# Performance work log

Hardware: AMD Instinct MI355X
Metric: run time of the kernel (lower is better)

Reference implementation:

```python
import jax, jax.numpy as jnp
import numpy as np

D = 2            # stalk dimension d
FD = 3           # final_d = d + 1 (add_lp=True, add_hp=False)
HID = 32         # hidden_channels
N_NODES = 50000
E0 = 200000      # undirected edges; directed edge list has 2*E0 entries (second half reversed)
IN_CH = 128
OUT_CH = 32
N_LAYERS = 2
PSIZE = D * (D + 1) // 2  # cayley param size per edge


def _spectral_normalize(W, iters=20):
    # torch spectral_norm: power iteration with detached u, v; sigma = u^T W v
    u = jnp.full((W.shape[0],), 1.0 / np.sqrt(W.shape[0]), W.dtype)
    def body(_, u):
        v = W.T @ u
        v = v / (jnp.linalg.norm(v) + 1e-12)
        u2 = W @ v
        return u2 / (jnp.linalg.norm(u2) + 1e-12)
    u = jax.lax.fori_loop(0, iters, body, u)
    u = jax.lax.stop_gradient(u)
    v = jax.lax.stop_gradient(W.T @ u)
    v = v / (jnp.linalg.norm(v) + 1e-12)
    return W / (u @ W @ v)


def _cayley(p):
    # p: [E, PSIZE] lower-tri params -> skew A -> orthogonal Q = (I - A)^{-1}(I + A)
    E = p.shape[0]
    r, c = jnp.tril_indices(D)
    M = jnp.zeros((E, D, D), p.dtype).at[:, r, c].set(p)
    A = M - jnp.swapaxes(M, 1, 2)
    I = jnp.eye(D, dtype=p.dtype)
    return jnp.linalg.solve(I[None] - A, I[None] + A)


def setup_inputs() -> dict:
    key = jax.random.key(0)
    ks = jax.random.split(key, 8)
    src = jax.random.randint(ks[0], (E0,), 0, N_NODES)
    dst = jax.random.randint(ks[1], (E0,), 0, N_NODES)
    # symmetric directed edge list; edge j and edge j+E0 are reverses of each other
    edge_index = jnp.concatenate([jnp.stack([src, dst]), jnp.stack([dst, src])], axis=1)
    x = jax.random.normal(ks[2], (N_NODES, IN_CH), jnp.float32)
    s = 0.02
    W1 = jax.random.normal(ks[3], (FD * HID, IN_CH), jnp.float32) * s
    b1 = jnp.zeros((FD * HID,), jnp.float32)
    W2 = jax.random.normal(ks[4], (OUT_CH, FD * HID), jnp.float32) * s
    b2 = jnp.zeros((OUT_CH,), jnp.float32)
    W_left = jnp.tile(jnp.eye(FD, dtype=jnp.float32)[None], (N_LAYERS, 1, 1))  # init eye per torch
    W_right = jax.random.normal(ks[5], (N_LAYERS, HID, HID), jnp.float32) / np.sqrt(HID)
    eps = jnp.zeros((N_LAYERS, FD, 1), jnp.float32)
    W_sheaf = jax.random.normal(ks[6], (N_LAYERS, PSIZE, 2 * FD * HID), jnp.float32) * s
    W_wt = jax.random.normal(ks[7], (N_LAYERS, 1, 2 * FD * HID), jnp.float32) * s
    return {"x": x, "edge_index": edge_index, "W1": W1, "b1": b1, "W2": W2, "b2": b2,
            "W_left": W_left, "W_right": W_right, "eps": eps, "W_sheaf": W_sheaf, "W_wt": W_wt}


def reference(x, edge_index, W1, b1, W2, b2, W_left, W_right, eps, W_sheaf, W_wt):
    N = x.shape[0]
    row, col = edge_index[0], edge_index[1]
    e0 = row.shape[0] // 2
    rev = jnp.concatenate([jnp.arange(e0) + e0, jnp.arange(e0)])  # reverse-edge index
    # lin1 + ELU (dropouts = 0 in eval)
    h = jax.nn.elu(x @ W1.T + b1)                 # [N, FD*HID]
    xc = h.reshape(N * FD, HID)                   # [N*FD, HID]
    x0 = xc
    for layer in range(N_LAYERS):
        # --- sheaf learner + edge weight learner (gather endpoint features) ---
        xn = xc.reshape(N, FD * HID)
        cat = jnp.concatenate([xn[row], xn[col]], axis=-1)   # [2*E0, 2*FD*HID]
        p = jnp.tanh(cat @ W_sheaf[layer].T)                 # sheaf map params [2*E0, PSIZE]
        wdir = jax.nn.sigmoid(cat @ W_wt[layer].T)[:, 0]
        w = wdir * wdir[rev]                                 # symmetric edge weight
        # --- normalized connection (bundle) Laplacian ---
        Q = _cayley(p)                                       # per-edge orthogonal maps
        T = jnp.einsum('eij,eik->ejk', Q, Q[rev])            # transport F_u^T F_v
        w2 = w * w
        deg = jax.ops.segment_sum(w2, row, num_segments=N)
        dinv = jnp.where(deg > 0, jax.lax.rsqrt(jnp.maximum(deg, 1e-30)), 0.0)
        cnorm = w2 * dinv[row] * dinv[col]                   # [2*E0]
        # --- left / right weights (spectral-normalized) ---
        Wl = _spectral_normalize(W_left[layer])
        Wr = _spectral_normalize(W_right[layer])
        y = xc.reshape(N, FD, HID)
        y = jnp.einsum('ef,nfh->neh', Wl, y)                 # mix stalk dims
        y = jnp.einsum('neh,ch->nec', y, Wr)                 # mix channels
        # --- apply block-sparse Laplacian: Lx[u] = x[u] - sum_e c_e B_e x[v] ---
        yv = y[col]                                          # gather  [2*E0, FD, HID]
        tv = jnp.concatenate([jnp.einsum('eij,ejh->eih', T, yv[:, :D]), yv[:, D:]], axis=1)
        agg = jax.ops.segment_sum(cnorm[:, None, None] * tv, row, num_segments=N)
        diag = jnp.where(deg > 0, 1.0, 0.0)[:, None, None]
        z = jax.nn.elu((diag * y - agg).reshape(N * FD, HID))
        # --- epsilon-gated residual ---
        coeff = jnp.tile(1.0 + jnp.tanh(eps[layer]), (N, 1))  # [N*FD, 1]
        x0 = coeff * x0 - z
        xc = x0
    return xc.reshape(N, FD * HID) @ W2.T + b2
```

## Files before the change

### kernel.cpp

```cpp
#include <hip/hip_runtime.h>
#include <hip/hip_bf16.h>

#define NN   50000
#define E0   200000
#define E2   400000

typedef __attribute__((ext_vector_type(8))) short short8;
typedef __attribute__((ext_vector_type(4))) float f32x4;

__device__ __forceinline__ float eluf(float x) { return x > 0.0f ? x : expm1f(x); }
__device__ __forceinline__ float sigmoidf(float x) { return 1.0f / (1.0f + expf(-x)); }
__device__ __forceinline__ unsigned rne_bf16(float x) {
    unsigned u = __float_as_uint(x);
    return (u + 0x7fffu + ((u >> 16) & 1u)) >> 16;
}

__global__ __launch_bounds__(256) void k_splitw(const float* __restrict__ W, int n,
                                                unsigned short* __restrict__ hi,
                                                unsigned short* __restrict__ lo) {
    int i = blockIdx.x * 256 + threadIdx.x;
    if (i >= n) return;
    float x = W[i];
    unsigned h = rne_bf16(x);
    hi[i] = (unsigned short)h;
    lo[i] = (unsigned short)rne_bf16(x - __uint_as_float(h << 16));
}

template<int K, int N, bool ELU>
__global__ __launch_bounds__(256) void k_gemm_mfma(const float* __restrict__ X,
                                                   const unsigned short* __restrict__ Whi,
                                                   const unsigned short* __restrict__ Wlo,
                                                   const float* __restrict__ bias,
                                                   float* __restrict__ out) {
    constexpr int KP = K + 8;
    constexpr int NT = N / 16;
    constexpr int KS = K / 32;
    __shared__ __align__(16) unsigned short whi[N * KP];
    __shared__ __align__(16) unsigned short wlo[N * KP];
    int tid = threadIdx.x;
    for (int i = tid; i < N * K / 2; i += 256) {
        unsigned vh = ((const unsigned*)Whi)[i];
        unsigned vl = ((const unsigned*)Wlo)[i];
        int e = i * 2, r = e / K, c = e % K;
        *(unsigned*)&whi[r * KP + c] = vh;
        *(unsigned*)&wlo[r * KP + c] = vl;
    }
    __syncthreads();
    int wave = tid >> 6, lane = tid & 63;
    int quad = lane >> 4, r16 = lane & 15;
    long m = (long)blockIdx.x * 64 + wave * 16 + r16;
    long mc = m < NN ? m : (NN - 1);
    const float* xrow = X + mc * K + quad * 8;
    f32x4 acc[NT];
#pragma unroll
    for (int t = 0; t < NT; ++t) acc[t] = (f32x4){0.f, 0.f, 0.f, 0.f};
#pragma unroll
    for (int ks = 0; ks < KS; ++ks) {
        const float4* xp = (const float4*)(xrow + ks * 32);
        float4 p0 = xp[0], p1 = xp[1];
        float xv[8] = {p0.x, p0.y, p0.z, p0.w, p1.x, p1.y, p1.z, p1.w};
        short8 a_hi, a_lo;
#pragma unroll
        for (int j = 0; j < 8; ++j) {
            unsigned h = rne_bf16(xv[j]);
            a_hi[j] = (short)h;
            a_lo[j] = (short)rne_bf16(xv[j] - __uint_as_float(h << 16));
        }
#pragma unroll
        for (int t = 0; t < NT; ++t) {
            int ro = (t * 16 + r16) * KP + ks * 32 + quad * 8;
            short8 bh = *(const short8*)&whi[ro];
            short8 bl = *(const short8*)&wlo[ro];
            acc[t] = __builtin_amdgcn_mfma_f32_16x16x32_bf16(a_hi, bh, acc[t], 0, 0, 0);
            acc[t] = __builtin_amdgcn_mfma_f32_16x16x32_bf16(a_lo, bh, acc[t], 0, 0, 0);
            acc[t] = __builtin_amdgcn_mfma_f32_16x16x32_bf16(a_hi, bl, acc[t], 0, 0, 0);
        }
    }
    long mbase = (long)blockIdx.x * 64 + wave * 16 + quad * 4;
#pragma unroll
    for (int t = 0; t < NT; ++t) {
        float b = bias[t * 16 + r16];
#pragma unroll
        for (int rr = 0; rr < 4; ++rr) {
            long mm = mbase + rr;
            if (mm < NN) {
                float v = acc[t][rr] + b;
                if (ELU) v = eluf(v);
                out[mm * N + t * 16 + r16] = v;
            }
        }
    }
}

__global__ __launch_bounds__(64) void k_spectral(const float* __restrict__ Wl_in,
                                                 const float* __restrict__ Wr_in,
                                                 float* __restrict__ Wl_out,
                                                 float* __restrict__ Wr_out) {
    int l = blockIdx.x, t = threadIdx.x;
    __shared__ float W[32 * 33];
    __shared__ float us[32], vs[32], tmp[32];
    __shared__ float scal;
    for (int i = t; i < 1024; i += 64) W[(i >> 5) * 33 + (i & 31)] = Wr_in[l * 1024 + i];
    if (t < 32) us[t] = 0.17677669529663688f;
    __syncthreads();
    for (int it = 0; it < 20; ++it) {
        if (t < 32) { float a = 0; for (int r = 0; r < 32; ++r) a = fmaf(W[r * 33 + t], us[r], a); tmp[t] = a; }
        __syncthreads();
        if (t == 0) { float s = 0; for (int c = 0; c < 32; ++c) s += tmp[c] * tmp[c]; scal = 1.0f / (sqrtf(s) + 1e-12f); }
        __syncthreads();
        if (t < 32) vs[t] = tmp[t] * scal;
        __syncthreads();
        if (t < 32) { float a = 0; for (int c = 0; c < 32; ++c) a = fmaf(W[t * 33 + c], vs[c], a); tmp[t] = a; }
        __syncthreads();
        if (t == 0) { float s = 0; for (int r = 0; r < 32; ++r) s += tmp[r] * tmp[r]; scal = 1.0f / (sqrtf(s) + 1e-12f); }
        __syncthreads();
        if (t < 32) us[t] = tmp[t] * scal;
        __syncthreads();
    }
    if (t < 32) { float a = 0; for (int r = 0; r < 32; ++r) a = fmaf(W[r * 33 + t], us[r], a); tmp[t] = a; }
    __syncthreads();
    if (t == 0) {
        float s = 0; for (int c = 0; c < 32; ++c) s += tmp[c] * tmp[c];
        scal = (sqrtf(s) + 1e-12f) / s;
    }
    __syncthreads();
    for (int i = t; i < 1024; i += 64) Wr_out[l * 1024 + i] = W[(i >> 5) * 33 + (i & 31)] * scal;

    if (t == 0) {
        float M[9];
        for (int i = 0; i < 9; ++i) M[i] = Wl_in[l * 9 + i];
        float u[3] = {0.5773502691896258f, 0.5773502691896258f, 0.5773502691896258f};
        float v[3], u2[3];
        for (int it = 0; it < 20; ++it) {
            float s = 0;
            for (int c = 0; c < 3; ++c) { v[c] = M[c] * u[0] + M[3 + c] * u[1] + M[6 + c] * u[2]; s += v[c] * v[c]; }
            float inv = 1.0f / (sqrtf(s) + 1e-12f);
            for (int c = 0; c < 3; ++c) v[c] *= inv;
            s = 0;
            for (int r = 0; r < 3; ++r) { u2[r] = M[r * 3] * v[0] + M[r * 3 + 1] * v[1] + M[r * 3 + 2] * v[2]; s += u2[r] * u2[r]; }
            inv = 1.0f / (sqrtf(s) + 1e-12f);
            for (int r = 0; r < 3; ++r) u[r] = u2[r] * inv;
        }
        float s = 0;
        for (int c = 0; c < 3; ++c) { v[c] = M[c] * u[0] + M[3 + c] * u[1] + M[6 + c] * u[2]; s += v[c] * v[c]; }
        float inv = (sqrtf(s) + 1e-12f) / s;
        for (int i = 0; i < 9; ++i) Wl_out[l * 9 + i] = M[i] * inv;
    }
}

__global__ __launch_bounds__(256) void k_hist(const int* __restrict__ row, int* __restrict__ cnt) {
    int e = blockIdx.x * 256 + threadIdx.x;
    if (e < E2) atomicAdd(&cnt[row[e]], 1);
}
__global__ __launch_bounds__(256) void k_scan1(const int* __restrict__ cnt, int* __restrict__ start,
                                               int* __restrict__ bsum) {
    __shared__ int s[256];
    int b = blockIdx.x, t = threadIdx.x;
    int i = b * 256 + t;
    int v = (i < NN) ? cnt[i] : 0;
    s[t] = v;
    __syncthreads();
    for (int off = 1; off < 256; off <<= 1) {
        int add = (t >= off) ? s[t - off] : 0;
        __syncthreads();
        s[t] += add;
        __syncthreads();
    }
    if (i < NN) start[i] = s[t] - v;
    if (t == 255) bsum[b] = s[t];
}
__global__ __launch_bounds__(256) void k_scan2(const int* __restrict__ bsum, int* __restrict__ bofs,
                                               int nb) {
    __shared__ int s[256];
    int t = threadIdx.x;
    int v = (t < nb) ? bsum[t] : 0;
    s[t] = v;
    __syncthreads();
    for (int off = 1; off < 256; off <<= 1) {
        int add = (t >= off) ? s[t - off] : 0;
        __syncthreads();
        s[t] += add;
        __syncthreads();
    }
    if (t < nb) bofs[t] = s[t] - v;
}
__global__ __launch_bounds__(256) void k_scan3(int* __restrict__ start, const int* __restrict__ bofs) {
    int i = blockIdx.x * 256 + threadIdx.x;
    if (i < NN) start[i] += bofs[i >> 8];
}
__global__ __launch_bounds__(256) void k_fill(const int* __restrict__ row, const int* __restrict__ start,
                                              int* __restrict__ fill, int* __restrict__ eslot) {
    int e = blockIdx.x * 256 + threadIdx.x;
    if (e >= E2) return;
    int u = row[e];
    eslot[e] = start[u] + atomicAdd(&fill[u], 1);
}

__global__ __launch_bounds__(256) void k_y8(const float* __restrict__ xc,
                                            const float* __restrict__ Wl,
                                            const float* __restrict__ Wr,
                                            const float* __restrict__ Wsh,
                                            const float* __restrict__ Wwt,
                                            int layer,
                                            unsigned* __restrict__ yp01,
                                            unsigned short* __restrict__ yp2,
                                            float* __restrict__ aR, float* __restrict__ aC,
                                            float* __restrict__ wR, float* __restrict__ wC,
                                            float* __restrict__ deg) {
    __shared__ float wrs[32 * 33];
    __shared__ float wls[9];
    __shared__ float xcs[8][96];
    __shared__ float ws1[192], wt[192];
    int tid = threadIdx.x;
    int n0 = blockIdx.x * 8;
    if (tid < 8) { int nz = n0 + tid; if (nz < NN) deg[nz] = 0.0f; }
    for (int i = tid; i < 1024; i += 256) wrs[(i >> 5) * 33 + (i & 31)] = Wr[i];
    if (tid < 9) wls[tid] = Wl[tid];
    if (tid < 192) {
        ws1[tid] = Wsh[(layer * 3 + 1) * 192 + tid];
        wt[tid]  = Wwt[layer * 192 + tid];
    }
    for (int i = tid; i < 768; i += 256) {
        int n = n0 + i / 96;
        xcs[i / 96][i % 96] = (n < NN) ? xc[n * 96 + i % 96] : 0.0f;
    }
    __syncthreads();
    int node = tid >> 5, c = tid & 31;
    int n = n0 + node;
    float a1 = 0, a2 = 0, a3 = 0, a4 = 0;
#pragma unroll
    for (int j = 0; j < 3; ++j) {
        int k = j * 32 + c;
        float xv = xcs[node][k];
        a1 = fmaf(xv, ws1[k], a1);
        a2 = fmaf(xv, ws1[96 + k], a2);
        a3 = fmaf(xv, wt[k], a3);
        a4 = fmaf(xv, wt[96 + k], a4);
    }
#pragma unroll
    for (int off = 16; off; off >>= 1) {
        a1 += __shfl_xor(a1, off);
        a2 += __shfl_xor(a2, off);
        a3 += __shfl_xor(a3, off);
        a4 += __shfl_xor(a4, off);
    }
    if (c == 0 && n < NN) { aR[n] = a1; aC[n] = a2; wR[n] = a3; wC[n] = a4; }
    if (n < NN) {
        float t0 = 0, t1 = 0, t2 = 0;
        const float* wr = &wrs[c * 33];
        const float* xr = xcs[node];
#pragma unroll
        for (int h = 0; h < 32; ++h) {
            float w = wr[h];
            t0 = fmaf(xr[h], w, t0);
            t1 = fmaf(xr[32 + h], w, t1);
            t2 = fmaf(xr[64 + h], w, t2);
        }
        float o0 = wls[0] * t0 + wls[1] * t1 + wls[2] * t2;
        float o1 = wls[3] * t0 + wls[4] * t1 + wls[5] * t2;
        float o2 = wls[6] * t0 + wls[7] * t1 + wls[8] * t2;
        yp01[n * 32 + c] = rne_bf16(o0) | (rne_bf16(o1) << 16);
        yp2[n * 32 + c]  = (unsigned short)rne_bf16(o2);
    }
}

__global__ __launch_bounds__(256) void k_edge_coef(const int* __restrict__ row, const int* __restrict__ col,
                                                   const int* __restrict__ eslot,
                                                   const float* __restrict__ aR, const float* __restrict__ aC,
                                                   const float* __restrict__ wR, const float* __restrict__ wC,
                                                   float4* __restrict__ meta, float* __restrict__ deg) {
    int e = blockIdx.x * 256 + threadIdx.x;
    if (e >= E0) return;
    int u = row[e], v = col[e];
    float a_e = tanhf(aR[u] + aC[v]);
    float a_r = tanhf(aR[v] + aC[u]);
    float wd_e = sigmoidf(wR[u] + wC[v]);
    float wd_r = sigmoidf(wR[v] + wC[u]);
    float w = wd_e * wd_r;
    float w2 = w * w;
    float ie = 1.0f / (1.0f + a_e * a_e), ir = 1.0f / (1.0f + a_r * a_r);
    float ce = (1.0f - a_e * a_e) * ie, se = 2.0f * a_e * ie;
    float cr = (1.0f - a_r * a_r) * ir, sr = 2.0f * a_r * ir;
    float C = ce * cr + se * sr;
    float S = ce * sr - se * cr;
    meta[eslot[e]]      = make_float4(C,  S, w2, __int_as_float(v));
    meta[eslot[e + E0]] = make_float4(C, -S, w2, __int_as_float(u));
    atomicAdd(&deg[u], w2);
    atomicAdd(&deg[v], w2);
}

__global__ __launch_bounds__(256) void k_dinv(const float* __restrict__ deg, float* __restrict__ dinv) {
    int n = blockIdx.x * 256 + threadIdx.x;
    if (n >= NN) return;
    float d = deg[n];
    dinv[n] = d > 0.0f ? rsqrtf(fmaxf(d, 1e-30f)) : 0.0f;
}

__global__ __launch_bounds__(256) void k_gather_update(const int* __restrict__ start, const int* __restrict__ cnt,
                                                       const float4* __restrict__ meta,
                                                       const float* __restrict__ dinv,
                                                       const unsigned* __restrict__ yp01,
                                                       const unsigned short* __restrict__ yp2,
                                                       const float* __restrict__ eps,
                                                       int layer, float* __restrict__ xc) {
    int tid = threadIdx.x;
    int node = tid >> 5, c = tid & 31;
    int n = blockIdx.x * 8 + node;
    if (n >= NN) return;
    int s0 = start[n], ec = cnt[n];
    float du = dinv[n];
    float acc0 = 0, acc1 = 0, acc2 = 0;
    for (int bs = 0; bs < ec; bs += 32) {
        int nb = min(32, ec - bs);
        float CC = 0, SS = 0, cnl = 0;
        int vj = 0;
        if (c < nb) {
            float4 mt = meta[s0 + bs + c];
            vj = __float_as_int(mt.w);
            cnl = mt.z * du * dinv[vj];
            CC = cnl * mt.x;
            SS = cnl * mt.y;
        }
        for (int j = 0; j < nb; ++j) {
            float Cj = __shfl(CC, j, 32);
            float Sj = __shfl(SS, j, 32);
            float cj = __shfl(cnl, j, 32);
            int v = __shfl(vj, j, 32);
            unsigned u01 = yp01[v * 32 + c];
            unsigned u2v = (unsigned)yp2[v * 32 + c];
            float y0 = __uint_as_float(u01 << 16);
            float y1 = __uint_as_float(u01 & 0xffff0000u);
            float y2 = __uint_as_float(u2v << 16);
            acc0 = fmaf(Cj, y0, acc0);
            acc0 = fmaf(-Sj, y1, acc0);
            acc1 = fmaf(Sj, y0, acc1);
            acc1 = fmaf(Cj, y1, acc1);
            acc2 = fmaf(cj, y2, acc2);
        }
    }
    float diag = du > 0.0f ? 1.0f : 0.0f;
    unsigned u01 = yp01[n * 32 + c];
    unsigned u2v = (unsigned)yp2[n * 32 + c];
    float oy0 = __uint_as_float(u01 << 16);
    float oy1 = __uint_as_float(u01 & 0xffff0000u);
    float oy2 = __uint_as_float(u2v << 16);
    float c0 = 1.0f + tanhf(eps[layer * 3 + 0]);
    float c1 = 1.0f + tanhf(eps[layer * 3 + 1]);
    float c2 = 1.0f + tanhf(eps[layer * 3 + 2]);
    int base = n * 96 + c;
    float z0 = eluf(diag * oy0 - acc0);
    float z1 = eluf(diag * oy1 - acc1);
    float z2 = eluf(diag * oy2 - acc2);
    xc[base]      = c0 * xc[base]      - z0;
    xc[base + 32] = c1 * xc[base + 32] - z1;
    xc[base + 64] = c2 * xc[base + 64] - z2;
}

extern "C" void kernel_launch(void* const* d_in, const int* in_sizes, int n_in,
                              void* d_out, int out_size, void* d_ws, size_t ws_size,
                              hipStream_t stream) {
    const float* x     = (const float*)d_in[0];
    const int*   ei    = (const int*)d_in[1];
    const float* W1    = (const float*)d_in[2];
    const float* b1    = (const float*)d_in[3];
    const float* W2    = (const float*)d_in[4];
    const float* bias2 = (const float*)d_in[5];
    const float* Wl_in = (const float*)d_in[6];
    const float* Wr_in = (const float*)d_in[7];
    const float* eps   = (const float*)d_in[8];
    const float* Wsh   = (const float*)d_in[9];
    const float* Wwt   = (const float*)d_in[10];
    float* out = (float*)d_out;
    const int* row = ei;
    const int* col = ei + E2;

    char* pc = (char*)d_ws;
    float* xc    = (float*)pc;          pc += (size_t)NN * 96 * 4;
    float4* meta = (float4*)pc;         pc += (size_t)E2 * 16;
    unsigned* yp01 = (unsigned*)pc;     pc += (size_t)NN * 32 * 4;
    unsigned short* yp2 = (unsigned short*)pc; pc += (size_t)NN * 32 * 2;
    float* aR    = (float*)pc;          pc += (size_t)NN * 4;
    float* aC    = (float*)pc;          pc += (size_t)NN * 4;
    float* wRp   = (float*)pc;          pc += (size_t)NN * 4;
    float* wCp   = (float*)pc;          pc += (size_t)NN * 4;
    float* deg   = (float*)pc;          pc += (size_t)NN * 4;
    float* dinv  = (float*)pc;          pc += (size_t)NN * 4;
    float* Wl_n  = (float*)pc;          pc += 32 * 4;
    float* Wr_n  = (float*)pc;          pc += 2048 * 4;
    int* cnt     = (int*)pc;            pc += (size_t)NN * 4;
    int* start   = (int*)pc;            pc += (size_t)NN * 4;
    int* fill    = (int*)pc;            pc += (size_t)NN * 4;
    int* eslot   = (int*)pc;            pc += (size_t)E2 * 4;
    int* bsum    = (int*)pc;            pc += 256 * 4;
    int* bofs    = (int*)pc;            pc += 256 * 4;
    unsigned short* w1hi = (unsigned short*)pc; pc += 96 * 128 * 2;
    unsigned short* w1lo = (unsigned short*)pc; pc += 96 * 128 * 2;
    unsigned short* w2hi = (unsigned short*)pc; pc += 32 * 96 * 2;
    unsigned short* w2lo = (unsigned short*)pc; pc += 32 * 96 * 2;

    const int NB  = (NN + 255) / 256;
    const int EB  = (E2 + 255) / 256;
    const int EB0 = (E0 + 255) / 256;
    const int MB  = (NN + 63) / 64;

    k_splitw<<<(96 * 128 + 255) / 256, 256, 0, stream>>>(W1, 96 * 128, w1hi, w1lo);
    k_splitw<<<(32 * 96 + 255) / 256, 256, 0, stream>>>(W2, 32 * 96, w2hi, w2lo);
    k_gemm_mfma<128, 96, true><<<MB, 256, 0, stream>>>(x, w1hi, w1lo, b1, xc);
    k_spectral<<<2, 64, 0, stream>>>(Wl_in, Wr_in, Wl_n, Wr_n);

    hipMemsetAsync(cnt, 0, NN * sizeof(int), stream);
    hipMemsetAsync(fill, 0, NN * sizeof(int), stream);
    k_hist<<<EB, 256, 0, stream>>>(row, cnt);
    k_scan1<<<NB, 256, 0, stream>>>(cnt, start, bsum);
    k_scan2<<<1, 256, 0, stream>>>(bsum, bofs, NB);
    k_scan3<<<NB, 256, 0, stream>>>(start, bofs);
    k_fill<<<EB, 256, 0, stream>>>(row, start, fill, eslot);

    for (int l = 0; l < 2; ++l) {
        k_y8<<<(NN + 7) / 8, 256, 0, stream>>>(xc, Wl_n + l * 9, Wr_n + l * 1024, Wsh, Wwt, l,
                                               yp01, yp2, aR, aC, wRp, wCp, deg);
        k_edge_coef<<<EB0, 256, 0, stream>>>(row, col, eslot, aR, aC, wRp, wCp, meta, deg);
        k_dinv<<<NB, 256, 0, stream>>>(deg, dinv);
        k_gather_update<<<(NN + 7) / 8, 256, 0, stream>>>(start, cnt, meta, dinv,
                                                          yp01, yp2, eps, l, xc);
    }
    k_gemm_mfma<96, 32, false><<<MB, 256, 0, stream>>>(xc, w2hi, w2lo, bias2, out);
}
```

Baseline: 377.6 us.

## Fuse all stages into one persistent cooperative kernel with grid syncs

Replaces the sequence of about 20 kernel launches (weight split, GEMMs, spectral norm, CSR build, per-layer edge/gather passes) with a single cooperative persistent kernel that separates the phases with grid.sync, and keeps the old multi-kernel path as a fallback. The aim is to remove launch overhead and inter-kernel gaps. The GEMM is restructured to stage 16-row weight slices in a shared-memory union, which adds block barriers and repeated weight loads per tile. Spectral normalisation is overlapped with the first GEMM on two dedicated blocks. Occupancy is capped by launch_bounds(256,4), and many grid-wide syncs plus reduced parallelism in some phases may offset the savings.

```diff
diff --git a/kernel.cpp b/kernel.cpp
--- a/kernel.cpp
+++ b/kernel.cpp
@@ -1,12 +1,17 @@
 #include <hip/hip_runtime.h>
-#include <hip/hip_bf16.h>
-
-#define NN   50000
-#define E0   200000
-#define E2   400000
+#include <hip/hip_cooperative_groups.h>
+
+#define NN 50000
+#define E0 200000
+#define E2 400000
+#define NGROUPS ((NN + 7) / 8)
+#define NCHUNK  ((NN + 255) / 256)
+#define NTILES  ((NN + 63) / 64)
 
 typedef __attribute__((ext_vector_type(8))) short short8;
 typedef __attribute__((ext_vector_type(4))) float f32x4;
+
+namespace cg = cooperative_groups;
 
 __device__ __forceinline__ float eluf(float x) { return x > 0.0f ? x : expm1f(x); }
 __device__ __forceinline__ float sigmoidf(float x) { return 1.0f / (1.0f + expf(-x)); }
@@ -15,117 +20,122 @@
     return (u + 0x7fffu + ((u >> 16) & 1u)) >> 16;
 }
 
-__global__ __launch_bounds__(256) void k_splitw(const float* __restrict__ W, int n,
-                                                unsigned short* __restrict__ hi,
-                                                unsigned short* __restrict__ lo) {
-    int i = blockIdx.x * 256 + threadIdx.x;
-    if (i >= n) return;
-    float x = W[i];
-    unsigned h = rne_bf16(x);
-    hi[i] = (unsigned short)h;
-    lo[i] = (unsigned short)rne_bf16(x - __uint_as_float(h << 16));
-}
+struct SMemGemm { unsigned short whi[16 * 136]; unsigned short wlo[16 * 136]; };
+struct SMemY8   { float wrs[32 * 33]; float wls[9]; float xcs[8][96]; float ws1[192]; float wt[192]; };
+struct SMemSpec { float W[32 * 33]; float us[32]; float vs[32]; float tmp[32]; float scal; };
+struct SMemScan { int s[256]; };
+union SMem { SMemGemm g; SMemY8 y; SMemSpec sp; SMemScan sc; };
+
+struct Params {
+    const float* x; const int* ei;
+    const float *W1, *b1, *W2, *b2, *Wl, *Wr, *eps, *Wsh, *Wwt;
+    float* out;
+    float* xc; float4* meta; unsigned* yp01; unsigned short* yp2;
+    float *aR, *aC, *wR, *wC, *deg, *dinv, *Wl_n, *Wr_n;
+    int *cnt, *start, *fill, *eslot, *bsum, *bofs;
+    unsigned short *w1hi, *w1lo, *w2hi, *w2lo;
+};
 
 template<int K, int N, bool ELU>
-__global__ __launch_bounds__(256) void k_gemm_mfma(const float* __restrict__ X,
-                                                   const unsigned short* __restrict__ Whi,
-                                                   const unsigned short* __restrict__ Wlo,
-                                                   const float* __restrict__ bias,
-                                                   float* __restrict__ out) {
+__device__ void gemm_phase(const float* __restrict__ X, const unsigned short* __restrict__ Whi,
+                           const unsigned short* __restrict__ Wlo, const float* __restrict__ bias,
+                           float* __restrict__ out, int bid, int nb, int tid, SMem* sm) {
     constexpr int KP = K + 8;
-    constexpr int NT = N / 16;
     constexpr int KS = K / 32;
-    __shared__ __align__(16) unsigned short whi[N * KP];
-    __shared__ __align__(16) unsigned short wlo[N * KP];
-    int tid = threadIdx.x;
-    for (int i = tid; i < N * K / 2; i += 256) {
-        unsigned vh = ((const unsigned*)Whi)[i];
-        unsigned vl = ((const unsigned*)Wlo)[i];
-        int e = i * 2, r = e / K, c = e % K;
-        *(unsigned*)&whi[r * KP + c] = vh;
-        *(unsigned*)&wlo[r * KP + c] = vl;
-    }
-    __syncthreads();
-    int wave = tid >> 6, lane = tid & 63;
-    int quad = lane >> 4, r16 = lane & 15;
-    long m = (long)blockIdx.x * 64 + wave * 16 + r16;
-    long mc = m < NN ? m : (NN - 1);
-    const float* xrow = X + mc * K + quad * 8;
-    f32x4 acc[NT];
-#pragma unroll
-    for (int t = 0; t < NT; ++t) acc[t] = (f32x4){0.f, 0.f, 0.f, 0.f};
-#pragma unroll
-    for (int ks = 0; ks < KS; ++ks) {
-        const float4* xp = (const float4*)(xrow + ks * 32);
-        float4 p0 = xp[0], p1 = xp[1];
-        float xv[8] = {p0.x, p0.y, p0.z, p0.w, p1.x, p1.y, p1.z, p1.w};
-        short8 a_hi, a_lo;
-#pragma unroll
-        for (int j = 0; j < 8; ++j) {
-            unsigned h = rne_bf16(xv[j]);
-            a_hi[j] = (short)h;
-            a_lo[j] = (short)rne_bf16(xv[j] - __uint_as_float(h << 16));
-        }
-#pragma unroll
-        for (int t = 0; t < NT; ++t) {
-            int ro = (t * 16 + r16) * KP + ks * 32 + quad * 8;
-            short8 bh = *(const short8*)&whi[ro];
-            short8 bl = *(const short8*)&wlo[ro];
-            acc[t] = __builtin_amdgcn_mfma_f32_16x16x32_bf16(a_hi, bh, acc[t], 0, 0, 0);
-            acc[t] = __builtin_amdgcn_mfma_f32_16x16x32_bf16(a_lo, bh, acc[t], 0, 0, 0);
-            acc[t] = __builtin_amdgcn_mfma_f32_16x16x32_bf16(a_hi, bl, acc[t], 0, 0, 0);
-        }
-    }
-    long mbase = (long)blockIdx.x * 64 + wave * 16 + quad * 4;
-#pragma unroll
-    for (int t = 0; t < NT; ++t) {
-        float b = bias[t * 16 + r16];
-#pragma unroll
-        for (int rr = 0; rr < 4; ++rr) {
-            long mm = mbase + rr;
-            if (mm < NN) {
-                float v = acc[t][rr] + b;
-                if (ELU) v = eluf(v);
-                out[mm * N + t * 16 + r16] = v;
-            }
-        }
-    }
-}
-
-__global__ __launch_bounds__(64) void k_spectral(const float* __restrict__ Wl_in,
-                                                 const float* __restrict__ Wr_in,
-                                                 float* __restrict__ Wl_out,
-                                                 float* __restrict__ Wr_out) {
-    int l = blockIdx.x, t = threadIdx.x;
-    __shared__ float W[32 * 33];
-    __shared__ float us[32], vs[32], tmp[32];
-    __shared__ float scal;
-    for (int i = t; i < 1024; i += 64) W[(i >> 5) * 33 + (i & 31)] = Wr_in[l * 1024 + i];
-    if (t < 32) us[t] = 0.17677669529663688f;
+    constexpr int CT = N / 32;
+    const int wave = tid >> 6, lane = tid & 63;
+    const int quad = lane >> 4, r16 = lane & 15;
+    for (int t = bid; t < NTILES; t += nb) {
+        long m = (long)t * 64 + wave * 16 + r16;
+        long mc = m < NN ? m : NN - 1;
+        const float* xrow = X + mc * K + quad * 8;
+        short8 ah[KS], al[KS];
+#pragma unroll
+        for (int ks = 0; ks < KS; ++ks) {
+            const float4* xp = (const float4*)(xrow + ks * 32);
+            float4 p0 = xp[0], p1 = xp[1];
+            float xv[8] = {p0.x, p0.y, p0.z, p0.w, p1.x, p1.y, p1.z, p1.w};
+#pragma unroll
+            for (int j = 0; j < 8; ++j) {
+                unsigned h = rne_bf16(xv[j]);
+                ah[ks][j] = (short)h;
+                al[ks][j] = (short)rne_bf16(xv[j] - __uint_as_float(h << 16));
+            }
+        }
+#pragma unroll
+        for (int ct = 0; ct < CT; ++ct) {
+            f32x4 accs[2];
+#pragma unroll
+            for (int sub = 0; sub < 2; ++sub) {
+                __syncthreads();
+                for (int i = tid; i < 16 * K / 2; i += 256) {
+                    int e = i * 2, r = e / K, c = e % K;
+                    int gp = (ct * 32 + sub * 16 + r) * (K / 2) + (c >> 1);
+                    unsigned vh = ((const unsigned*)Whi)[gp];
+                    unsigned vl = ((const unsigned*)Wlo)[gp];
+                    *(unsigned*)&sm->g.whi[r * KP + c] = vh;
+                    *(unsigned*)&sm->g.wlo[r * KP + c] = vl;
+                }
+                __syncthreads();
+                f32x4 a0 = {0.f, 0.f, 0.f, 0.f};
+#pragma unroll
+                for (int ks = 0; ks < KS; ++ks) {
+                    int ro = r16 * KP + ks * 32 + quad * 8;
+                    short8 bh = *(const short8*)&sm->g.whi[ro];
+                    short8 bl = *(const short8*)&sm->g.wlo[ro];
+                    a0 = __builtin_amdgcn_mfma_f32_16x16x32_bf16(ah[ks], bh, a0, 0, 0, 0);
+                    a0 = __builtin_amdgcn_mfma_f32_16x16x32_bf16(al[ks], bh, a0, 0, 0, 0);
+                    a0 = __builtin_amdgcn_mfma_f32_16x16x32_bf16(ah[ks], bl, a0, 0, 0, 0);
+                }
+                accs[sub] = a0;
+            }
+            long mbase = (long)t * 64 + wave * 16 + quad * 4;
+#pragma unroll
+            for (int tt = 0; tt < 2; ++tt) {
+                float b = bias[ct * 32 + tt * 16 + r16];
+#pragma unroll
+                for (int rr = 0; rr < 4; ++rr) {
+                    long mm = mbase + rr;
+                    if (mm < NN) {
+                        float v = accs[tt][rr] + b;
+                        if (ELU) v = eluf(v);
+                        out[mm * N + ct * 32 + tt * 16 + r16] = v;
+                    }
+                }
+            }
+        }
+    }
+}
+
+__device__ void spectral_dev(int l, int t, const float* __restrict__ Wl_in,
+                             const float* __restrict__ Wr_in,
+                             float* __restrict__ Wl_out, float* __restrict__ Wr_out, SMem* sm) {
+    SMemSpec& S = sm->sp;
+    for (int i = t; i < 1024; i += 256) S.W[(i >> 5) * 33 + (i & 31)] = Wr_in[l * 1024 + i];
+    if (t < 32) S.us[t] = 0.17677669529663688f;
     __syncthreads();
     for (int it = 0; it < 20; ++it) {
-        if (t < 32) { float a = 0; for (int r = 0; r < 32; ++r) a = fmaf(W[r * 33 + t], us[r], a); tmp[t] = a; }
-        __syncthreads();
-        if (t == 0) { float s = 0; for (int c = 0; c < 32; ++c) s += tmp[c] * tmp[c]; scal = 1.0f / (sqrtf(s) + 1e-12f); }
-        __syncthreads();
-        if (t < 32) vs[t] = tmp[t] * scal;
-        __syncthreads();
-        if (t < 32) { float a = 0; for (int c = 0; c < 32; ++c) a = fmaf(W[t * 33 + c], vs[c], a); tmp[t] = a; }
-        __syncthreads();
-        if (t == 0) { float s = 0; for (int r = 0; r < 32; ++r) s += tmp[r] * tmp[r]; scal = 1.0f / (sqrtf(s) + 1e-12f); }
-        __syncthreads();
-        if (t < 32) us[t] = tmp[t] * scal;
-        __syncthreads();
-    }
-    if (t < 32) { float a = 0; for (int r = 0; r < 32; ++r) a = fmaf(W[r * 33 + t], us[r], a); tmp[t] = a; }
+        if (t < 32) { float a = 0; for (int r = 0; r < 32; ++r) a = fmaf(S.W[r * 33 + t], S.us[r], a); S.tmp[t] = a; }
+        __syncthreads();
+        if (t == 0) { float s = 0; for (int c = 0; c < 32; ++c) s += S.tmp[c] * S.tmp[c]; S.scal = 1.0f / (sqrtf(s) + 1e-12f); }
+        __syncthreads();
+        if (t < 32) S.vs[t] = S.tmp[t] * S.scal;
+        __syncthreads();
+        if (t < 32) { float a = 0; for (int c = 0; c < 32; ++c) a = fmaf(S.W[t * 33 + c], S.vs[c], a); S.tmp[t] = a; }
+        __syncthreads();
+        if (t == 0) { float s = 0; for (int r = 0; r < 32; ++r) s += S.tmp[r] * S.tmp[r]; S.scal = 1.0f / (sqrtf(s) + 1e-12f); }
+        __syncthreads();
+        if (t < 32) S.us[t] = S.tmp[t] * S.scal;
+        __syncthreads();
+    }
+    if (t < 32) { float a = 0; for (int r = 0; r < 32; ++r) a = fmaf(S.W[r * 33 + t], S.us[r], a); S.tmp[t] = a; }
     __syncthreads();
     if (t == 0) {
-        float s = 0; for (int c = 0; c < 32; ++c) s += tmp[c] * tmp[c];
-        scal = (sqrtf(s) + 1e-12f) / s;
+        float s = 0; for (int c = 0; c < 32; ++c) s += S.tmp[c] * S.tmp[c];
+        S.scal = (sqrtf(s) + 1e-12f) / s;
     }
     __syncthreads();
-    for (int i = t; i < 1024; i += 64) Wr_out[l * 1024 + i] = W[(i >> 5) * 33 + (i & 31)] * scal;
-
+    for (int i = t; i < 1024; i += 256) Wr_out[l * 1024 + i] = S.W[(i >> 5) * 33 + (i & 31)] * S.scal;
     if (t == 0) {
         float M[9];
         for (int i = 0; i < 9; ++i) M[i] = Wl_in[l * 9 + i];
@@ -148,11 +158,260 @@
     }
 }
 
-__global__ __launch_bounds__(256) void k_hist(const int* __restrict__ row, int* __restrict__ cnt) {
+__global__ __launch_bounds__(256, 4) void k_mega(Params p) {
+    cg::grid_group grid = cg::this_grid();
+    const int tid = threadIdx.x;
+    const int bid = blockIdx.x;
+    const int G = gridDim.x;
+    const int gtid = bid * 256 + tid;
+    const int GT = G * 256;
+    __shared__ SMem sm;
+    const int* row = p.ei;
+    const int* col = p.ei + E2;
+
+    for (int i = gtid; i < 96 * 128; i += GT) {
+        float v = p.W1[i];
+        unsigned h = rne_bf16(v);
+        p.w1hi[i] = (unsigned short)h;
+        p.w1lo[i] = (unsigned short)rne_bf16(v - __uint_as_float(h << 16));
+    }
+    for (int i = gtid; i < 32 * 96; i += GT) {
+        float v = p.W2[i];
+        unsigned h = rne_bf16(v);
+        p.w2hi[i] = (unsigned short)h;
+        p.w2lo[i] = (unsigned short)rne_bf16(v - __uint_as_float(h << 16));
+    }
+    for (int i = gtid; i < NN; i += GT) { p.cnt[i] = 0; p.fill[i] = 0; p.deg[i] = 0.0f; }
+    grid.sync();
+
+    if (bid < 2) {
+        spectral_dev(bid, tid, p.Wl, p.Wr, p.Wl_n, p.Wr_n, &sm);
+    } else {
+        gemm_phase<128, 96, true>(p.x, p.w1hi, p.w1lo, p.b1, p.xc, bid - 2, G - 2, tid, &sm);
+        for (int e = (bid - 2) * 256 + tid; e < E2; e += (G - 2) * 256)
+            atomicAdd(&p.cnt[row[e]], 1);
+    }
+    grid.sync();
+
+    for (int ch = bid; ch < NCHUNK; ch += G) {
+        int i = ch * 256 + tid;
+        int v = (i < NN) ? p.cnt[i] : 0;
+        sm.sc.s[tid] = v;
+        __syncthreads();
+        for (int off = 1; off < 256; off <<= 1) {
+            int add = (tid >= off) ? sm.sc.s[tid - off] : 0;
+            __syncthreads();
+            sm.sc.s[tid] += add;
+            __syncthreads();
+        }
+        if (i < NN) p.start[i] = sm.sc.s[tid] - v;
+        if (tid == 255) p.bsum[ch] = sm.sc.s[255];
+        __syncthreads();
+    }
+    grid.sync();
+
+    if (bid == 0) {
+        int v = (tid < NCHUNK) ? p.bsum[tid] : 0;
+        sm.sc.s[tid] = v;
+        __syncthreads();
+        for (int off = 1; off < 256; off <<= 1) {
+            int add = (tid >= off) ? sm.sc.s[tid - off] : 0;
+            __syncthreads();
+            sm.sc.s[tid] += add;
+            __syncthreads();
+        }
+        if (tid < NCHUNK) p.bofs[tid] = sm.sc.s[tid] - v;
+    }
+    grid.sync();
+
+    for (int i = gtid; i < NN; i += GT) p.start[i] += p.bofs[i >> 8];
+    grid.sync();
+
+    for (int e = gtid; e < E2; e += GT) {
+        int u = row[e];
+        p.eslot[e] = p.start[u] + atomicAdd(&p.fill[u], 1);
+    }
+    grid.sync();
+
+    for (int l = 0; l < 2; ++l) {
+        for (int i = gtid; i < NN; i += GT) p.deg[i] = 0.0f;
+        for (int i = tid; i < 1024; i += 256) sm.y.wrs[(i >> 5) * 33 + (i & 31)] = p.Wr_n[l * 1024 + i];
+        if (tid < 9) sm.y.wls[tid] = p.Wl_n[l * 9 + tid];
+        if (tid < 192) {
+            sm.y.ws1[tid] = p.Wsh[(l * 3 + 1) * 192 + tid];
+            sm.y.wt[tid]  = p.Wwt[l * 192 + tid];
+        }
+        for (int gi = bid; gi < NGROUPS; gi += G) {
+            int n0 = gi * 8;
+            __syncthreads();
+            for (int i = tid; i < 768; i += 256) {
+                int n = n0 + i / 96;
+                sm.y.xcs[i / 96][i % 96] = (n < NN) ? p.xc[n * 96 + i % 96] : 0.0f;
+            }
+            __syncthreads();
+            int node = tid >> 5, c = tid & 31;
+            int n = n0 + node;
+            float a1 = 0, a2 = 0, a3 = 0, a4 = 0;
+#pragma unroll
+            for (int j = 0; j < 3; ++j) {
+                int k = j * 32 + c;
+                float xv = sm.y.xcs[node][k];
+                a1 = fmaf(xv, sm.y.ws1[k], a1);
+                a2 = fmaf(xv, sm.y.ws1[96 + k], a2);
+                a3 = fmaf(xv, sm.y.wt[k], a3);
+                a4 = fmaf(xv, sm.y.wt[96 + k], a4);
+            }
+#pragma unroll
+            for (int off = 16; off; off >>= 1) {
+                a1 += __shfl_xor(a1, off);
+                a2 += __shfl_xor(a2, off);
+                a3 += __shfl_xor(a3, off);
+                a4 += __shfl_xor(a4, off);
+            }
+            if (c == 0 && n < NN) { p.aR[n] = a1; p.aC[n] = a2; p.wR[n] = a3; p.wC[n] = a4; }
+            if (n < NN) {
+                float t0 = 0, t1 = 0, t2 = 0;
+                const float* wr = &sm.y.wrs[c * 33];
+                const float* xr = sm.y.xcs[node];
+#pragma unroll
+                for (int h = 0; h < 32; ++h) {
+                    float w = wr[h];
+                    t0 = fmaf(xr[h], w, t0);
+                    t1 = fmaf(xr[32 + h], w, t1);
+                    t2 = fmaf(xr[64 + h], w, t2);
+                }
+                float o0 = sm.y.wls[0] * t0 + sm.y.wls[1] * t1 + sm.y.wls[2] * t2;
+                float o1 = sm.y.wls[3] * t0 + sm.y.wls[4] * t1 + sm.y.wls[5] * t2;
+                float o2 = sm.y.wls[6] * t0 + sm.y.wls[7] * t1 + sm.y.wls[8] * t2;
+                p.yp01[n * 32 + c] = rne_bf16(o0) | (rne_bf16(o1) << 16);
+                p.yp2[n * 32 + c]  = (unsigned short)rne_bf16(o2);
+            }
+        }
+        grid.sync();
+
+        for (int e = gtid; e < E0; e += GT) {
+            int u = row[e], v = col[e];
+            float a_e = tanhf(p.aR[u] + p.aC[v]);
+            float a_r = tanhf(p.aR[v] + p.aC[u]);
+            float wd_e = sigmoidf(p.wR[u] + p.wC[v]);
+            float wd_r = sigmoidf(p.wR[v] + p.wC[u]);
+            float w = wd_e * wd_r;
+            float w2 = w * w;
+            float ie = 1.0f / (1.0f + a_e * a_e), ir = 1.0f / (1.0f + a_r * a_r);
+            float ce = (1.0f - a_e * a_e) * ie, se = 2.0f * a_e * ie;
+            float cr = (1.0f - a_r * a_r) * ir, sr = 2.0f * a_r * ir;
+            float C = ce * cr + se * sr;
+            float S = ce * sr - se * cr;
+            p.meta[p.eslot[e]]      = make_float4(C,  S, w2, __int_as_float(v));
+            p.meta[p.eslot[e + E0]] = make_float4(C, -S, w2, __int_as_float(u));
+            atomicAdd(&p.deg[u], w2);
+            atomicAdd(&p.deg[v], w2);
+        }
+        grid.sync();
+
+        for (int i = gtid; i < NN; i += GT) {
+            float d = p.deg[i];
+            p.dinv[i] = d > 0.0f ? rsqrtf(fmaxf(d, 1e-30f)) : 0.0f;
+        }
+        grid.sync();
+
+        for (int gi = bid; gi < NGROUPS; gi += G) {
+            int node = tid >> 5, c = tid & 31;
+            int n = gi * 8 + node;
+            if (n < NN) {
+                int s0 = p.start[n], ec = p.cnt[n];
+                float du = p.dinv[n];
+                float acc0 = 0, acc1 = 0, acc2 = 0;
+                for (int bs = 0; bs < ec; bs += 32) {
+                    int nb2 = min(32, ec - bs);
+                    float CC = 0, SS = 0, cnl = 0;
+                    int vj = 0;
+                    if (c < nb2) {
+                        float4 mt = p.meta[s0 + bs + c];
+                        vj = __float_as_int(mt.w);
+                        cnl = mt.z * du * p.dinv[vj];
+                        CC = cnl * mt.x;
+                        SS = cnl * mt.y;
+                    }
+                    for (int j = 0; j < nb2; ++j) {
+                        float Cj = __shfl(CC, j, 32);
+                        float Sj = __shfl(SS, j, 32);
+                        float cj = __shfl(cnl, j, 32);
+                        int v = __shfl(vj, j, 32);
+                        unsigned u01 = p.yp01[v * 32 + c];
+                        unsigned u2v = (unsigned)p.yp2[v * 32 + c];
+                        float y0 = __uint_as_float(u01 << 16);
+                        float y1 = __uint_as_float(u01 & 0xffff0000u);
+                        float y2 = __uint_as_float(u2v << 16);
+                        acc0 = fmaf(Cj, y0, acc0);
+                        acc0 = fmaf(-Sj, y1, acc0);
+                        acc1 = fmaf(Sj, y0, acc1);
+                        acc1 = fmaf(Cj, y1, acc1);
+                        acc2 = fmaf(cj, y2, acc2);
+                    }
+                }
+                float diag = du > 0.0f ? 1.0f : 0.0f;
+                unsigned u01 = p.yp01[n * 32 + c];
+                unsigned u2v = (unsigned)p.yp2[n * 32 + c];
+                float oy0 = __uint_as_float(u01 << 16);
+                float oy1 = __uint_as_float(u01 & 0xffff0000u);
+                float oy2 = __uint_as_float(u2v << 16);
+                float c0 = 1.0f + tanhf(p.eps[l * 3 + 0]);
+                float c1 = 1.0f + tanhf(p.eps[l * 3 + 1]);
+                float c2 = 1.0f + tanhf(p.eps[l * 3 + 2]);
+                int base = n * 96 + c;
+                float z0 = eluf(diag * oy0 - acc0);
+                float z1 = eluf(diag * oy1 - acc1);
+                float z2 = eluf(diag * oy2 - acc2);
+                p.xc[base]      = c0 * p.xc[base]      - z0;
+                p.xc[base + 32] = c1 * p.xc[base + 32] - z1;
+                p.xc[base + 64] = c2 * p.xc[base + 64] - z2;
+            }
+        }
+        grid.sync();
+    }
+
+    gemm_phase<96, 32, false>(p.xc, p.w2hi, p.w2lo, p.b2, p.out, bid, G, tid, &sm);
+}
+
+__global__ __launch_bounds__(256) void f_splitw(const float* __restrict__ W, int n,
+                                                unsigned short* __restrict__ hi,
+                                                unsigned short* __restrict__ lo) {
+    int i = blockIdx.x * 256 + threadIdx.x;
+    if (i >= n) return;
+    float x = W[i];
+    unsigned h = rne_bf16(x);
+    hi[i] = (unsigned short)h;
+    lo[i] = (unsigned short)rne_bf16(x - __uint_as_float(h << 16));
+}
+
+template<int K, int N, bool ELU>
+__global__ __launch_bounds__(256) void f_gemm(const float* __restrict__ X,
+                                              const unsigned short* __restrict__ Whi,
+                                              const unsigned short* __restrict__ Wlo,
+                                              const float* __restrict__ bias,
+                                              float* __restrict__ out) {
+    __shared__ SMem sm;
+    gemm_phase<K, N, ELU>(X, Whi, Wlo, bias, out, blockIdx.x, gridDim.x, threadIdx.x, &sm);
+}
+
+__global__ __launch_bounds__(256) void f_spectral(const float* __restrict__ Wl_in,
+                                                  const float* __restrict__ Wr_in,
+                                                  float* __restrict__ Wl_out,
+                                                  float* __restrict__ Wr_out) {
+    __shared__ SMem sm;
+    spectral_dev(blockIdx.x, threadIdx.x, Wl_in, Wr_in, Wl_out, Wr_out, &sm);
+}
+
+__global__ __launch_bounds__(256) void f_zero(int* cnt, int* fill, float* deg) {
+    int i = blockIdx.x * 256 + threadIdx.x;
+    if (i < NN) { cnt[i] = 0; fill[i] = 0; deg[i] = 0.0f; }
+}
+__global__ __launch_bounds__(256) void f_hist(const int* __restrict__ row, int* __restrict__ cnt) {
     int e = blockIdx.x * 256 + threadIdx.x;
     if (e < E2) atomicAdd(&cnt[row[e]], 1);
 }
-__global__ __launch_bounds__(256) void k_scan1(const int* __restrict__ cnt, int* __restrict__ start,
+__global__ __launch_bounds__(256) void f_scan1(const int* __restrict__ cnt, int* __restrict__ start,
                                                int* __restrict__ bsum) {
     __shared__ int s[256];
     int b = blockIdx.x, t = threadIdx.x;
@@ -169,8 +428,7 @@
     if (i < NN) start[i] = s[t] - v;
     if (t == 255) bsum[b] = s[t];
 }
-__global__ __launch_bounds__(256) void k_scan2(const int* __restrict__ bsum, int* __restrict__ bofs,
-                                               int nb) {
+__global__ __launch_bounds__(256) void f_scan2(const int* __restrict__ bsum, int* __restrict__ bofs, int nb) {
     __shared__ int s[256];
     int t = threadIdx.x;
     int v = (t < nb) ? bsum[t] : 0;
@@ -184,11 +442,11 @@
     }
     if (t < nb) bofs[t] = s[t] - v;
 }
-__global__ __launch_bounds__(256) void k_scan3(int* __restrict__ start, const int* __restrict__ bofs) {
+__global__ __launch_bounds__(256) void f_scan3(int* __restrict__ start, const int* __restrict__ bofs) {
     int i = blockIdx.x * 256 + threadIdx.x;
     if (i < NN) start[i] += bofs[i >> 8];
 }
-__global__ __launch_bounds__(256) void k_fill(const int* __restrict__ row, const int* __restrict__ start,
+__global__ __launch_bounds__(256) void f_fill(const int* __restrict__ row, const int* __restrict__ start,
                                               int* __restrict__ fill, int* __restrict__ eslot) {
     int e = blockIdx.x * 256 + threadIdx.x;
     if (e >= E2) return;
@@ -196,33 +454,28 @@
     eslot[e] = start[u] + atomicAdd(&fill[u], 1);
 }
 
-__global__ __launch_bounds__(256) void k_y8(const float* __restrict__ xc,
-                                            const float* __restrict__ Wl,
-                                            const float* __restrict__ Wr,
-                                            const float* __restrict__ Wsh,
-                                            const float* __restrict__ Wwt,
-                                            int layer,
-                                            unsigned* __restrict__ yp01,
+__global__ __launch_bounds__(256) void f_y8(const float* __restrict__ xc,
+                                            const float* __restrict__ Wl, const float* __restrict__ Wr,
+                                            const float* __restrict__ Wsh, const float* __restrict__ Wwt,
+                                            int layer, unsigned* __restrict__ yp01,
                                             unsigned short* __restrict__ yp2,
                                             float* __restrict__ aR, float* __restrict__ aC,
                                             float* __restrict__ wR, float* __restrict__ wC,
                                             float* __restrict__ deg) {
-    __shared__ float wrs[32 * 33];
-    __shared__ float wls[9];
-    __shared__ float xcs[8][96];
-    __shared__ float ws1[192], wt[192];
+    __shared__ SMem smu;
+    SMemY8& sy = smu.y;
     int tid = threadIdx.x;
     int n0 = blockIdx.x * 8;
     if (tid < 8) { int nz = n0 + tid; if (nz < NN) deg[nz] = 0.0f; }
-    for (int i = tid; i < 1024; i += 256) wrs[(i >> 5) * 33 + (i & 31)] = Wr[i];
-    if (tid < 9) wls[tid] = Wl[tid];
+    for (int i = tid; i < 1024; i += 256) sy.wrs[(i >> 5) * 33 + (i & 31)] = Wr[i];
+    if (tid < 9) sy.wls[tid] = Wl[tid];
     if (tid < 192) {
-        ws1[tid] = Wsh[(layer * 3 + 1) * 192 + tid];
-        wt[tid]  = Wwt[layer * 192 + tid];
+        sy.ws1[tid] = Wsh[(layer * 3 + 1) * 192 + tid];
+        sy.wt[tid]  = Wwt[layer * 192 + tid];
     }
     for (int i = tid; i < 768; i += 256) {
         int n = n0 + i / 96;
-        xcs[i / 96][i % 96] = (n < NN) ? xc[n * 96 + i % 96] : 0.0f;
+        sy.xcs[i / 96][i % 96] = (n < NN) ? xc[n * 96 + i % 96] : 0.0f;
     }
     __syncthreads();
     int node = tid >> 5, c = tid & 31;
@@ -231,11 +484,11 @@
 #pragma unroll
     for (int j = 0; j < 3; ++j) {
         int k = j * 32 + c;
-        float xv = xcs[node][k];
-        a1 = fmaf(xv, ws1[k], a1);
-        a2 = fmaf(xv, ws1[96 + k], a2);
-        a3 = fmaf(xv, wt[k], a3);
-        a4 = fmaf(xv, wt[96 + k], a4);
+        float xv = sy.xcs[node][k];
+        a1 = fmaf(xv, sy.ws1[k], a1);
+        a2 = fmaf(xv, sy.ws1[96 + k], a2);
+        a3 = fmaf(xv, sy.wt[k], a3);
+        a4 = fmaf(xv, sy.wt[96 + k], a4);
     }
 #pragma unroll
     for (int off = 16; off; off >>= 1) {
@@ -247,8 +500,8 @@
     if (c == 0 && n < NN) { aR[n] = a1; aC[n] = a2; wR[n] = a3; wC[n] = a4; }
     if (n < NN) {
         float t0 = 0, t1 = 0, t2 = 0;
-        const float* wr = &wrs[c * 33];
-        const float* xr = xcs[node];
+        const float* wr = &sy.wrs[c * 33];
+        const float* xr = sy.xcs[node];
 #pragma unroll
         for (int h = 0; h < 32; ++h) {
             float w = wr[h];
@@ -256,19 +509,19 @@
             t1 = fmaf(xr[32 + h], w, t1);
             t2 = fmaf(xr[64 + h], w, t2);
         }
-        float o0 = wls[0] * t0 + wls[1] * t1 + wls[2] * t2;
-        float o1 = wls[3] * t0 + wls[4] * t1 + wls[5] * t2;
-        float o2 = wls[6] * t0 + wls[7] * t1 + wls[8] * t2;
+        float o0 = sy.wls[0] * t0 + sy.wls[1] * t1 + sy.wls[2] * t2;
+        float o1 = sy.wls[3] * t0 + sy.wls[4] * t1 + sy.wls[5] * t2;
+        float o2 = sy.wls[6] * t0 + sy.wls[7] * t1 + sy.wls[8] * t2;
         yp01[n * 32 + c] = rne_bf16(o0) | (rne_bf16(o1) << 16);
         yp2[n * 32 + c]  = (unsigned short)rne_bf16(o2);
     }
 }
 
-__global__ __launch_bounds__(256) void k_edge_coef(const int* __restrict__ row, const int* __restrict__ col,
-                                                   const int* __restrict__ eslot,
-                                                   const float* __restrict__ aR, const float* __restrict__ aC,
-                                                   const float* __restrict__ wR, const float* __restrict__ wC,
-                                                   float4* __restrict__ meta, float* __restrict__ deg) {
+__global__ __launch_bounds__(256) void f_coef(const int* __restrict__ row, const int* __restrict__ col,
+                                              const int* __restrict__ eslot,
+                                              const float* __restrict__ aR, const float* __restrict__ aC,
+                                              const float* __restrict__ wR, const float* __restrict__ wC,
+                                              float4* __restrict__ meta, float* __restrict__ deg) {
     int e = blockIdx.x * 256 + threadIdx.x;
     if (e >= E0) return;
     int u = row[e], v = col[e];
@@ -289,20 +542,20 @@
     atomicAdd(&deg[v], w2);
 }
 
-__global__ __launch_bounds__(256) void k_dinv(const float* __restrict__ deg, float* __restrict__ dinv) {
+__global__ __launch_bounds__(256) void f_dinv(const float* __restrict__ deg, float* __restrict__ dinv) {
     int n = blockIdx.x * 256 + threadIdx.x;
     if (n >= NN) return;
     float d = deg[n];
     dinv[n] = d > 0.0f ? rsqrtf(fmaxf(d, 1e-30f)) : 0.0f;
 }
 
-__global__ __launch_bounds__(256) void k_gather_update(const int* __restrict__ start, const int* __restrict__ cnt,
-                                                       const float4* __restrict__ meta,
-                                                       const float* __restrict__ dinv,
-                                                       const unsigned* __restrict__ yp01,
-                                                       const unsigned short* __restrict__ yp2,
-                                                       const float* __restrict__ eps,
-                                                       int layer, float* __restrict__ xc) {
+__global__ __launch_bounds__(256) void f_gather(const int* __restrict__ start, const int* __restrict__ cnt,
+                                                const float4* __restrict__ meta,
+                                                const float* __restrict__ dinv,
+                                                const unsigned* __restrict__ yp01,
+                                                const unsigned short* __restrict__ yp2,
+                                                const float* __restrict__ eps,
+                                                int layer, float* __restrict__ xc) {
     int tid = threadIdx.x;
     int node = tid >> 5, c = tid & 31;
     int n = blockIdx.x * 8 + node;
@@ -311,17 +564,17 @@
     float du = dinv[n];
     float acc0 = 0, acc1 = 0, acc2 = 0;
     for (int bs = 0; bs < ec; bs += 32) {
-        int nb = min(32, ec - bs);
+        int nb2 = min(32, ec - bs);
         float CC = 0, SS = 0, cnl = 0;
         int vj = 0;
-        if (c < nb) {
+        if (c < nb2) {
             float4 mt = meta[s0 + bs + c];
             vj = __float_as_int(mt.w);
             cnl = mt.z * du * dinv[vj];
             CC = cnl * mt.x;
             SS = cnl * mt.y;
         }
-        for (int j = 0; j < nb; ++j) {
+        for (int j = 0; j < nb2; ++j) {
             float Cj = __shfl(CC, j, 32);
             float Sj = __shfl(SS, j, 32);
             float cj = __shfl(cnl, j, 32);
@@ -359,70 +612,84 @@
 extern "C" void kernel_launch(void* const* d_in, const int* in_sizes, int n_in,
                               void* d_out, int out_size, void* d_ws, size_t ws_size,
                               hipStream_t stream) {
-    const float* x     = (const float*)d_in[0];
-    const int*   ei    = (const int*)d_in[1];
-    const float* W1    = (const float*)d_in[2];
-    const float* b1    = (const float*)d_in[3];
-    const float* W2    = (const float*)d_in[4];
-    const float* bias2 = (const float*)d_in[5];
-    const float* Wl_in = (const float*)d_in[6];
-    const float* Wr_in = (const float*)d_in[7];
-    const float* eps   = (const float*)d_in[8];
-    const float* Wsh   = (const float*)d_in[9];
-    const float* Wwt   = (const float*)d_in[10];
-    float* out = (float*)d_out;
-    const int* row = ei;
-    const int* col = ei + E2;
+    Params p;
+    p.x   = (const float*)d_in[0];
+    p.ei  = (const int*)d_in[1];
+    p.W1  = (const float*)d_in[2];
+    p.b1  = (const float*)d_in[3];
+    p.W2  = (const float*)d_in[4];
+    p.b2  = (const float*)d_in[5];
+    p.Wl  = (const float*)d_in[6];
+    p.Wr  = (const float*)d_in[7];
+    p.eps = (const float*)d_in[8];
+    p.Wsh = (const float*)d_in[9];
+    p.Wwt = (const float*)d_in[10];
+    p.out = (float*)d_out;
 
     char* pc = (char*)d_ws;
-    float* xc    = (float*)pc;          pc += (size_t)NN * 96 * 4;
-    float4* meta = (float4*)pc;         pc += (size_t)E2 * 16;
-    unsigned* yp01 = (unsigned*)pc;     pc += (size_t)NN * 32 * 4;
-    unsigned short* yp2 = (unsigned short*)pc; pc += (size_t)NN * 32 * 2;
-    float* aR    = (float*)pc;          pc += (size_t)NN * 4;
-    float* aC    = (float*)pc;          pc += (size_t)NN * 4;
-    float* wRp   = (float*)pc;          pc += (size_t)NN * 4;
-    float* wCp   = (float*)pc;          pc += (size_t)NN * 4;
-    float* deg   = (float*)pc;          pc += (size_t)NN * 4;
-    float* dinv  = (float*)pc;          pc += (size_t)NN * 4;
-    float* Wl_n  = (float*)pc;          pc += 32 * 4;
-    float* Wr_n  = (float*)pc;          pc += 2048 * 4;
-    int* cnt     = (int*)pc;            pc += (size_t)NN * 4;
-    int* start   = (int*)pc;            pc += (size_t)NN * 4;
-    int* fill    = (int*)pc;            pc += (size_t)NN * 4;
-    int* eslot   = (int*)pc;            pc += (size_t)E2 * 4;
-    int* bsum    = (int*)pc;            pc += 256 * 4;
-    int* bofs    = (int*)pc;            pc += 256 * 4;
-    unsigned short* w1hi = (unsigned short*)pc; pc += 96 * 128 * 2;
-    unsigned short* w1lo = (unsigned short*)pc; pc += 96 * 128 * 2;
-    unsigned short* w2hi = (unsigned short*)pc; pc += 32 * 96 * 2;
-    unsigned short* w2lo = (unsigned short*)pc; pc += 32 * 96 * 2;
-
-    const int NB  = (NN + 255) / 256;
-    const int EB  = (E2 + 255) / 256;
-    const int EB0 = (E0 + 255) / 256;
-    const int MB  = (NN + 63) / 64;
-
-    k_splitw<<<(96 * 128 + 255) / 256, 256, 0, stream>>>(W1, 96 * 128, w1hi, w1lo);
-    k_splitw<<<(32 * 96 + 255) / 256, 256, 0, stream>>>(W2, 32 * 96, w2hi, w2lo);
-    k_gemm_mfma<128, 96, true><<<MB, 256, 0, stream>>>(x, w1hi, w1lo, b1, xc);
-    k_spectral<<<2, 64, 0, stream>>>(Wl_in, Wr_in, Wl_n, Wr_n);
-
-    hipMemsetAsync(cnt, 0, NN * sizeof(int), stream);
-    hipMemsetAsync(fill, 0, NN * sizeof(int), stream);
-    k_hist<<<EB, 256, 0, stream>>>(row, cnt);
-    k_scan1<<<NB, 256, 0, stream>>>(cnt, start, bsum);
-    k_scan2<<<1, 256, 0, stream>>>(bsum, bofs, NB);
-    k_scan3<<<NB, 256, 0, stream>>>(start, bofs);
-    k_fill<<<EB, 256, 0, stream>>>(row, start, fill, eslot);
-
-    for (int l = 0; l < 2; ++l) {
-        k_y8<<<(NN + 7) / 8, 256, 0, stream>>>(xc, Wl_n + l * 9, Wr_n + l * 1024, Wsh, Wwt, l,
-                                               yp01, yp2, aR, aC, wRp, wCp, deg);
-        k_edge_coef<<<EB0, 256, 0, stream>>>(row, col, eslot, aR, aC, wRp, wCp, meta, deg);
-        k_dinv<<<NB, 256, 0, stream>>>(deg, dinv);
-        k_gather_update<<<(NN + 7) / 8, 256, 0, stream>>>(start, cnt, meta, dinv,
-                                                          yp01, yp2, eps, l, xc);
-    }
-    k_gemm_mfma<96, 32, false><<<MB, 256, 0, stream>>>(xc, w2hi, w2lo, bias2, out);
-}
+    p.xc    = (float*)pc;            pc += (size_t)NN * 96 * 4;
+    p.meta  = (float4*)pc;           pc += (size_t)E2 * 16;
+    p.yp01  = (unsigned*)pc;         pc += (size_t)NN * 32 * 4;
+    p.yp2   = (unsigned short*)pc;   pc += (size_t)NN * 32 * 2;
+    pc = (char*)(((size_t)pc + 15) & ~(size_t)15);
+    p.aR    = (float*)pc;            pc += (size_t)NN * 4;
+    p.aC    = (float*)pc;            pc += (size_t)NN * 4;
+    p.wR    = (float*)pc;            pc += (size_t)NN * 4;
+    p.wC    = (float*)pc;            pc += (size_t)NN * 4;
+    p.deg   = (float*)pc;            pc += (size_t)NN * 4;
+    p.dinv  = (float*)pc;            pc += (size_t)NN * 4;
+    p.Wl_n  = (float*)pc;            pc += 32 * 4;
+    p.Wr_n  = (float*)pc;            pc += 2048 * 4;
+    p.cnt   = (int*)pc;              pc += (size_t)NN * 4;
+    p.start = (int*)pc;              pc += (size_t)NN * 4;
+    p.fill  = (int*)pc;              pc += (size_t)NN * 4;
+    p.eslot = (int*)pc;              pc += (size_t)E2 * 4;
+    p.bsum  = (int*)pc;              pc += 256 * 4;
+    p.bofs  = (int*)pc;              pc += 256 * 4;
+    p.w1hi  = (unsigned short*)pc;   pc += 96 * 128 * 2;
+    p.w1lo  = (unsigned short*)pc;   pc += 96 * 128 * 2;
+    p.w2hi  = (unsigned short*)pc;   pc += 32 * 96 * 2;
+    p.w2lo  = (unsigned short*)pc;   pc += 32 * 96 * 2;
+
+    int occ = 0;
+    hipError_t qerr = hipOccupancyMaxActiveBlocksPerMultiprocessor(&occ, (const void*)k_mega, 256, 0);
+    int nCU = 256;
+    {
+        hipDeviceProp_t prop;
+        int dev = 0;
+        if (hipGetDevice(&dev) == hipSuccess && hipGetDeviceProperties(&prop, dev) == hipSuccess)
+            nCU = prop.multiProcessorCount;
+    }
+    long gridN = (qerr == hipSuccess && occ > 0) ? (long)occ * nCU : 0;
+    if (gridN > 2048) gridN = 2048;
+
+    hipError_t lerr = hipErrorUnknown;
+    if (gridN >= 3) {
+        void* args[] = { &p };
+        lerr = hipLaunchCooperativeKernel((void*)k_mega, dim3((unsigned)gridN), dim3(256), args, 0, stream);
+    }
+    if (lerr != hipSuccess) {
+        const int NB  = (NN + 255) / 256;
+        const int EB  = (E2 + 255) / 256;
+        const int EB0 = (E0 + 255) / 256;
+        f_splitw<<<(96 * 128 + 255) / 256, 256, 0, stream>>>(p.W1, 96 * 128, p.w1hi, p.w1lo);
+        f_splitw<<<(32 * 96 + 255) / 256, 256, 0, stream>>>(p.W2, 32 * 96, p.w2hi, p.w2lo);
+        f_gemm<128, 96, true><<<NTILES, 256, 0, stream>>>(p.x, p.w1hi, p.w1lo, p.b1, p.xc);
+        f_spectral<<<2, 256, 0, stream>>>(p.Wl, p.Wr, p.Wl_n, p.Wr_n);
+        f_zero<<<NB, 256, 0, stream>>>(p.cnt, p.fill, p.deg);
+        f_hist<<<EB, 256, 0, stream>>>(p.ei, p.cnt);
+        f_scan1<<<NB, 256, 0, stream>>>(p.cnt, p.start, p.bsum);
+        f_scan2<<<1, 256, 0, stream>>>(p.bsum, p.bofs, NB);
+        f_scan3<<<NB, 256, 0, stream>>>(p.start, p.bofs);
+        f_fill<<<EB, 256, 0, stream>>>(p.ei, p.start, p.fill, p.eslot);
+        for (int l = 0; l < 2; ++l) {
+            f_y8<<<NGROUPS, 256, 0, stream>>>(p.xc, p.Wl_n + l * 9, p.Wr_n + l * 1024, p.Wsh, p.Wwt, l,
+                                              p.yp01, p.yp2, p.aR, p.aC, p.wR, p.wC, p.deg);
+            f_coef<<<EB0, 256, 0, stream>>>(p.ei, p.ei + E2, p.eslot, p.aR, p.aC, p.wR, p.wC, p.meta, p.deg);
+            f_dinv<<<NB, 256, 0, stream>>>(p.deg, p.dinv);
+            f_gather<<<NGROUPS, 256, 0, stream>>>(p.start, p.cnt, p.meta, p.dinv,
+                                                  p.yp01, p.yp2, p.eps, l, p.xc);
+        }
+        f_gemm<96, 32, false><<<NTILES, 256, 0, stream>>>(p.xc, p.w2hi, p.w2lo, p.b2, p.out);
+    }
+}
```

New measurement: 1.006 ms. 166% more time.
